# Performance work log

Hardware: AMD Instinct MI355X
Metric: run time of the kernel (lower is better)

## Reference

```python
import jax, jax.numpy as jnp
import numpy as np

H = 8        # heads
R = 8        # rank of Lambda
WWIN = 8     # topk window w
T = 2        # num_iterations


def _rotate_half(x):
    h = x.shape[-1] // 2
    return jnp.concatenate([-x[..., h:], x[..., :h]], axis=-1)


def _gelu(x):
    return jax.nn.gelu(x, approximate=False)  # torch nn.GELU default is exact erf


def _forward(target, context, Wt, bt, Wc, bc, Ws1, bs1, Ws2, bs2,
             Wa1, ba1, Wa2, ba2, Wl1, bl1, Wl2, bl2, step_sizes, Wo, bo):
    B, L, D = target.shape
    K = context.shape[1]
    HD = D // H
    u = (target @ Wt + bt).reshape(B, L, H, HD).transpose(0, 2, 1, 3)   # [B,H,L,HD]
    v = (context @ Wc + bc).reshape(B, K, H, HD).transpose(0, 2, 1, 3)  # [B,H,K,HD]

    # scored-window connectivity: first scorer layer is separable over concat([t_i, c_j])
    h1 = (target @ Ws1[:D])[:, :, None, :] + (context @ Ws1[D:])[:, None, :, :] + bs1  # [B,L,K,EH]
    scores = (_gelu(h1) @ Ws2 + bs2)[..., 0]                                           # [B,L,K]
    _, idx = jax.lax.top_k(scores, WWIN)                                               # [B,L,w]
    E = L * WWIN
    edge_j = idx.reshape(B, E)
    edge_i = jnp.broadcast_to(jnp.repeat(jnp.arange(L), WWIN)[None], (B, E))

    # per-edge learnable params R_ij = alpha_ij I + Lambda_ij Lambda_ij^T
    tf = jnp.take_along_axis(target, edge_i[..., None], axis=1)   # [B,E,D]
    cf = jnp.take_along_axis(context, edge_j[..., None], axis=1)  # [B,E,D]
    ef = jnp.concatenate([tf, cf], axis=-1)                       # [B,E,2D]
    alphas = jax.nn.softplus(_gelu(ef @ Wa1 + ba1) @ Wa2 + ba2)[..., 0]     # [B,E]
    Lam = (_gelu(ef @ Wl1 + bl1) @ Wl2 + bl2).reshape(B, E, H, R, HD)
    Lam = Lam / jnp.maximum(jnp.linalg.norm(Lam, axis=-1, keepdims=True), 1e-12)

    # relative-position rotary applied to gathered target states (model_type='SC')
    inv_freq = 1.0 / (10000.0 ** (jnp.arange(0, HD, 2, dtype=jnp.float32) / HD))
    ang = (edge_i - edge_j).astype(jnp.float32)[..., None] * inv_freq       # [B,E,HD/2]
    cos = jnp.concatenate([jnp.cos(ang), jnp.cos(ang)], -1)[:, None]        # [B,1,E,HD]
    sin = jnp.concatenate([jnp.sin(ang), jnp.sin(ang)], -1)[:, None]

    def scatter_edges(res_b, ei_b):  # res_b [H,E,HD] -> [H,L,HD]
        return jax.ops.segment_sum(res_b.transpose(1, 0, 2), ei_b,
                                   num_segments=L).transpose(1, 0, 2)

    for t in range(T):
        step = jax.nn.softplus(step_sizes[t])[None, None, :, None]          # [1,1,L,1] (max_len == L)
        u_i = jnp.take_along_axis(u, edge_i[:, None, :, None], axis=2)      # [B,H,E,HD]
        u_i = u_i * cos + _rotate_half(u_i) * sin
        v_j = jnp.take_along_axis(v, edge_j[:, None, :, None], axis=2)      # [B,H,E,HD]
        diff = u_i - v_j
        Ld = jnp.einsum('behrd,bhed->bher', Lam, diff)                      # [B,H,E,R]
        residual = alphas[:, None, :, None] * diff + jnp.einsum('bher,behrd->bhed', Ld, Lam)
        u = u - step * jax.vmap(scatter_edges)(residual, edge_i)

    y = u.transpose(0, 2, 1, 3).reshape(B, L, D) @ Wo + bo  # dropout is identity in eval
    return y


def setup_inputs() -> dict:
    key = jax.random.key(0)
    B, L, K, D, EH = 2, 2048, 2048, 512, 16
    HD = D // H
    ks = iter(jax.random.split(key, 24))

    def lin(i, o):
        return jax.random.normal(next(ks), (i, o), jnp.float32) * (1.0 / float(np.sqrt(i)))

    def bias(o):
        return jnp.zeros((o,), jnp.float32)

    return {
        'target': jax.random.normal(next(ks), (B, L, D), jnp.float32),
        'context': jax.random.normal(next(ks), (B, K, D), jnp.float32),
        'Wt': lin(D, D), 'bt': bias(D),
        'Wc': lin(D, D), 'bc': bias(D),
        'Ws1': lin(2 * D, EH), 'bs1': bias(EH),
        'Ws2': lin(EH, 1), 'bs2': bias(1),
        'Wa1': lin(2 * D, EH), 'ba1': bias(EH),
        'Wa2': lin(EH, 1), 'ba2': bias(1),
        'Wl1': lin(2 * D, EH), 'bl1': bias(EH),
        'Wl2': lin(EH, H * R * HD), 'bl2': bias(H * R * HD),
        'step_sizes': jnp.full((T, L), -2.2, jnp.float32),
        'Wo': lin(D, D), 'bo': bias(D),
    }


def reference(target, context, Wt, bt, Wc, bc, Ws1, bs1, Ws2, bs2,
              Wa1, ba1, Wa2, ba2, Wl1, bl1, Wl2, bl2, step_sizes, Wo, bo):
    return _forward(target, context, Wt, bt, Wc, bc, Ws1, bs1, Ws2, bs2,
                    Wa1, ba1, Wa2, ba2, Wl1, bl1, Wl2, bl2, step_sizes, Wo, bo)
```

## Files before the change

### kernel.cpp

```cpp
#include <hip/hip_runtime.h>
#include <math.h>

#define BB 2
#define LL 2048
#define KK 2048
#define DD 512
#define HH 8
#define HD_ 64
#define RR 8
#define WWIN 8
#define NE (LL * WWIN)

typedef __attribute__((ext_vector_type(8))) short bf16x8s;
typedef __attribute__((ext_vector_type(4))) float f32x4;

__device__ __forceinline__ float gelu_f(float x) {
    return 0.5f * x * (1.0f + erff(x * 0.70710678118654752f));
}
__device__ __forceinline__ float softplus_f(float x) {
    return (x > 20.0f) ? x : log1pf(expf(x));
}
__device__ __forceinline__ unsigned short f2bf(float f) {
    unsigned int x = __float_as_uint(f);
    x += 0x7FFFu + ((x >> 16) & 1u);
    return (unsigned short)(x >> 16);
}
__device__ __forceinline__ float bf2f(unsigned short s) {
    return __uint_as_float(((unsigned int)s) << 16);
}

#define GEMM_SMEM_BYTES 15360

__device__ __forceinline__ void gemm_bf16_body(
    const float* __restrict__ A, const float* __restrict__ W,
    const float* __restrict__ bias, float* __restrict__ C,
    int M, int N, int Kd, int bx, int by, char* smem) {
    short (*As)[40] = (short(*)[40])smem;
    short (*Bs)[40] = (short(*)[40])(smem + 128 * 40 * 2);
    const int tid = threadIdx.x;
    const int m0 = bx * 128, n0 = by * 64;
    const int wv = tid >> 6, lane = tid & 63;
    const int wm = (wv & 1) << 6, wn = (wv >> 1) << 5;
    const int l15 = lane & 15, lg = lane >> 4;

    f32x4 acc[4][2] = {};
    union S8 { bf16x8s v; short s[8]; };

    const int arow = tid >> 1, akh = (tid & 1) << 4;
    const int bk = tid >> 3, bnb = (tid & 7) << 3;

    for (int k0 = 0; k0 < Kd; k0 += 32) {
        {
            const float* ap = &A[(size_t)(m0 + arow) * Kd + k0 + akh];
            float4 f0 = *(const float4*)(ap + 0);
            float4 f1 = *(const float4*)(ap + 4);
            float4 f2 = *(const float4*)(ap + 8);
            float4 f3 = *(const float4*)(ap + 12);
            S8 s0, s1;
            s0.s[0] = f2bf(f0.x); s0.s[1] = f2bf(f0.y); s0.s[2] = f2bf(f0.z); s0.s[3] = f2bf(f0.w);
            s0.s[4] = f2bf(f1.x); s0.s[5] = f2bf(f1.y); s0.s[6] = f2bf(f1.z); s0.s[7] = f2bf(f1.w);
            s1.s[0] = f2bf(f2.x); s1.s[1] = f2bf(f2.y); s1.s[2] = f2bf(f2.z); s1.s[3] = f2bf(f2.w);
            s1.s[4] = f2bf(f3.x); s1.s[5] = f2bf(f3.y); s1.s[6] = f2bf(f3.z); s1.s[7] = f2bf(f3.w);
            *(bf16x8s*)&As[arow][akh] = s0.v;
            *(bf16x8s*)&As[arow][akh + 8] = s1.v;
        }
        {
            const float* wp = &W[(size_t)(k0 + bk) * N + n0 + bnb];
            float4 w0 = *(const float4*)(wp + 0);
            float4 w1 = *(const float4*)(wp + 4);
            Bs[bnb + 0][bk] = f2bf(w0.x);
            Bs[bnb + 1][bk] = f2bf(w0.y);
            Bs[bnb + 2][bk] = f2bf(w0.z);
            Bs[bnb + 3][bk] = f2bf(w0.w);
            Bs[bnb + 4][bk] = f2bf(w1.x);
            Bs[bnb + 5][bk] = f2bf(w1.y);
            Bs[bnb + 6][bk] = f2bf(w1.z);
            Bs[bnb + 7][bk] = f2bf(w1.w);
        }
        __syncthreads();
        bf16x8s af[4], bf[2];
#pragma unroll
        for (int mf = 0; mf < 4; ++mf)
            af[mf] = *(const bf16x8s*)&As[wm + (mf << 4) + l15][lg << 3];
#pragma unroll
        for (int nf = 0; nf < 2; ++nf)
            bf[nf] = *(const bf16x8s*)&Bs[wn + (nf << 4) + l15][lg << 3];
#pragma unroll
        for (int mf = 0; mf < 4; ++mf)
#pragma unroll
            for (int nf = 0; nf < 2; ++nf)
                acc[mf][nf] = __builtin_amdgcn_mfma_f32_16x16x32_bf16(af[mf], bf[nf], acc[mf][nf], 0, 0, 0);
        __syncthreads();
    }
    float bv[2] = {0.f, 0.f};
    if (bias) {
        bv[0] = bias[n0 + wn + l15];
        bv[1] = bias[n0 + wn + 16 + l15];
    }
#pragma unroll
    for (int mf = 0; mf < 4; ++mf)
#pragma unroll
        for (int nf = 0; nf < 2; ++nf)
#pragma unroll
            for (int j = 0; j < 4; ++j) {
                int crow = m0 + wm + (mf << 4) + (lg << 2) + j;
                int ccol = n0 + wn + (nf << 4) + l15;
                C[(size_t)crow * N + ccol] = acc[mf][nf][j] + bv[nf];
            }
}

__device__ __forceinline__ void gemm_f32_body(
    const float* __restrict__ A, const float* __restrict__ W,
    float* __restrict__ C, int M, int N, int Kd, int bx, int by, char* smem) {
    float (*As)[68] = (float(*)[68])smem;
    float (*Bs)[68] = (float(*)[68])(smem + 16 * 68 * 4);
    const int tid = threadIdx.x;
    const int m0 = bx * 64, n0 = by * 64;
    const int tx = tid & 15, ty = tid >> 4;
    const int row_a = tid >> 2, kq_a = (tid & 3) << 2;
    const int kw = tid >> 4, nq = (tid & 15) << 2;
    float acc[4][4] = {};
    for (int k0 = 0; k0 < Kd; k0 += 16) {
        float4 av = *(const float4*)&A[(size_t)(m0 + row_a) * Kd + k0 + kq_a];
        As[kq_a + 0][row_a] = av.x;
        As[kq_a + 1][row_a] = av.y;
        As[kq_a + 2][row_a] = av.z;
        As[kq_a + 3][row_a] = av.w;
        *(float4*)&Bs[kw][nq] = *(const float4*)&W[(size_t)(k0 + kw) * N + n0 + nq];
        __syncthreads();
#pragma unroll
        for (int k = 0; k < 16; ++k) {
            float4 a4 = *(const float4*)&As[k][ty << 2];
            float4 b4 = *(const float4*)&Bs[k][tx << 2];
            acc[0][0] = fmaf(a4.x, b4.x, acc[0][0]);
            acc[0][1] = fmaf(a4.x, b4.y, acc[0][1]);
            acc[0][2] = fmaf(a4.x, b4.z, acc[0][2]);
            acc[0][3] = fmaf(a4.x, b4.w, acc[0][3]);
            acc[1][0] = fmaf(a4.y, b4.x, acc[1][0]);
            acc[1][1] = fmaf(a4.y, b4.y, acc[1][1]);
            acc[1][2] = fmaf(a4.y, b4.z, acc[1][2]);
            acc[1][3] = fmaf(a4.y, b4.w, acc[1][3]);
            acc[2][0] = fmaf(a4.z, b4.x, acc[2][0]);
            acc[2][1] = fmaf(a4.z, b4.y, acc[2][1]);
            acc[2][2] = fmaf(a4.z, b4.z, acc[2][2]);
            acc[2][3] = fmaf(a4.z, b4.w, acc[2][3]);
            acc[3][0] = fmaf(a4.w, b4.x, acc[3][0]);
            acc[3][1] = fmaf(a4.w, b4.y, acc[3][1]);
            acc[3][2] = fmaf(a4.w, b4.z, acc[3][2]);
            acc[3][3] = fmaf(a4.w, b4.w, acc[3][3]);
        }
        __syncthreads();
    }
#pragma unroll
    for (int q = 0; q < 4; ++q) {
        float4 o;
        o.x = acc[q][0];
        o.y = acc[q][1];
        o.z = acc[q][2];
        o.w = acc[q][3];
        *(float4*)&C[(size_t)(m0 + (ty << 2) + q) * N + n0 + (tx << 2)] = o;
    }
}

__global__ __launch_bounds__(256) void gemms_all(
    const float* __restrict__ target, const float* __restrict__ context,
    const float* __restrict__ Wt, const float* __restrict__ bt,
    const float* __restrict__ Wc, const float* __restrict__ bc,
    const float* __restrict__ wct, const float* __restrict__ wcc,
    float* __restrict__ u, float* __restrict__ v,
    float* __restrict__ t64, float* __restrict__ c64) {
    __shared__ __align__(16) char smem[GEMM_SMEM_BYTES];
    const int bid = blockIdx.x;
    if (bid < 64) {
        gemm_f32_body(target, wct, t64, 4096, 64, 512, bid, 0, smem);
    } else if (bid < 128) {
        gemm_f32_body(context, wcc, c64, 4096, 64, 512, bid - 64, 0, smem);
    } else if (bid < 384) {
        const int r = bid - 128;
        gemm_bf16_body(target, Wt, bt, u, 4096, 512, 512, r & 31, r >> 5, smem);
    } else {
        const int r = bid - 384;
        gemm_bf16_body(context, Wc, bc, v, 4096, 512, 512, r & 31, r >> 5, smem);
    }
}

__global__ __launch_bounds__(256) void gemm_bf16(
    const float* __restrict__ A, const float* __restrict__ W,
    const float* __restrict__ bias, float* __restrict__ C,
    int M, int N, int Kd) {
    __shared__ __align__(16) char smem[GEMM_SMEM_BYTES];
    gemm_bf16_body(A, W, bias, C, M, N, Kd, blockIdx.x, blockIdx.y, smem);
}

__global__ void prep_all(const float* __restrict__ Ws1, const float* __restrict__ Wa1,
                         const float* __restrict__ Wl1,
                         const float* __restrict__ Wl2, const float* __restrict__ bl2,
                         float* __restrict__ Wct, float* __restrict__ Wcc,
                         unsigned short* __restrict__ wl2bfT,
                         float* __restrict__ rot) {
    if (blockIdx.x < 128) {
        int idx = blockIdx.x * 256 + threadIdx.x;
        int k = idx >> 6, c = idx & 63;
        float vt = 0.f, vc = 0.f;
        if (c < 16)      { vt = Ws1[k * 16 + c];        vc = Ws1[(512 + k) * 16 + c]; }
        else if (c < 32) { vt = Wa1[k * 16 + (c - 16)]; vc = Wa1[(512 + k) * 16 + (c - 16)]; }
        else if (c < 48) { vt = Wl1[k * 16 + (c - 32)]; vc = Wl1[(512 + k) * 16 + (c - 32)]; }
        Wct[idx] = vt;
        Wcc[idx] = vc;
    } else if (blockIdx.x < 144) {
        int c = (blockIdx.x - 128) * 256 + threadIdx.x;
        union U8 { bf16x8s v; unsigned short s[8]; } r0, r1, r2, r3;
#pragma unroll
        for (int k = 0; k < 8; ++k) r0.s[k] = f2bf(Wl2[(size_t)k * 4096 + c]);
#pragma unroll
        for (int k = 0; k < 8; ++k) r1.s[k] = f2bf(Wl2[(size_t)(k + 8) * 4096 + c]);
#pragma unroll
        for (int k = 0; k < 8; ++k) { r2.s[k] = 0; r3.s[k] = 0; }
        r2.s[0] = f2bf(bl2[c]);
        unsigned short* dst = &wl2bfT[(size_t)c * 32];
        *(bf16x8s*)(dst + 0)  = r0.v;
        *(bf16x8s*)(dst + 8)  = r1.v;
        *(bf16x8s*)(dst + 16) = r2.v;
        *(bf16x8s*)(dst + 24) = r3.v;
    } else {
        int idx = (blockIdx.x - 144) * 256 + threadIdx.x;
        int dlt = (idx >> 5) - 2047;
        int k = idx & 31;
        float invf = exp2f((float)k * (-13.287712379549449f / 32.0f));
        float s, c;
        sincosf((float)dlt * invf, &s, &c);
        ((float2*)rot)[idx] = make_float2(c, s);
    }
}

__global__ __launch_bounds__(256) void scores_topk(
    const float* __restrict__ t64, const float* __restrict__ c64,
    const float* __restrict__ bs1, const float* __restrict__ Ws2,
    const float* __restrict__ bs2, int* __restrict__ edge_j) {
    __shared__ float sc[KK];
    __shared__ float wvs[4];
    __shared__ int wvj[4];
    const int tid = threadIdx.x;
    const int b = blockIdx.x >> 11;
    const int i = blockIdx.x & (LL - 1);
    float tsb[16], w2[16];
    const float* tr = &t64[(size_t)(b * LL + i) * 64];
#pragma unroll
    for (int k = 0; k < 16; ++k) { tsb[k] = tr[k] + bs1[k]; w2[k] = Ws2[k]; }
    const float b2 = bs2[0];
    for (int j = tid; j < KK; j += 256) {
        const float4* cr4 = (const float4*)&c64[(size_t)(b * KK + j) * 64];
        float creg[16];
        float4 c0 = cr4[0], c1 = cr4[1], c2 = cr4[2], c3 = cr4[3];
        creg[0] = c0.x; creg[1] = c0.y; creg[2] = c0.z; creg[3] = c0.w;
        creg[4] = c1.x; creg[5] = c1.y; creg[6] = c1.z; creg[7] = c1.w;
        creg[8] = c2.x; creg[9] = c2.y; creg[10] = c2.z; creg[11] = c2.w;
        creg[12] = c3.x; creg[13] = c3.y; creg[14] = c3.z; creg[15] = c3.w;
        float s = b2;
#pragma unroll
        for (int k = 0; k < 16; ++k)
            s = fmaf(gelu_f(tsb[k] + creg[k]), w2[k], s);
        sc[j] = s;
    }
    __syncthreads();

    float ls[8];
#pragma unroll
    for (int k = 0; k < 8; ++k) ls[k] = sc[tid + (k << 8)];
    const int lane = tid & 63, wv = tid >> 6;
#pragma unroll
    for (int w = 0; w < WWIN; ++w) {
        float cs = ls[0];
        int ck = 0;
#pragma unroll
        for (int k = 1; k < 8; ++k)
            if (ls[k] > cs) { cs = ls[k]; ck = k; }
        int cj = tid + (ck << 8);
#pragma unroll
        for (int m = 1; m < 64; m <<= 1) {
            float os = __shfl_xor(cs, m);
            int oj = __shfl_xor(cj, m);
            if (os > cs || (os == cs && oj < cj)) { cs = os; cj = oj; }
        }
        if (lane == 0) { wvs[wv] = cs; wvj[wv] = cj; }
        __syncthreads();
        float bsv = wvs[0];
        int bjv = wvj[0];
#pragma unroll
        for (int q = 1; q < 4; ++q) {
            float qs = wvs[q];
            int qj = wvj[q];
            if (qs > bsv || (qs == bsv && qj < bjv)) { bsv = qs; bjv = qj; }
        }
        if (tid == 0) edge_j[(size_t)(b * LL + i) * WWIN + w] = bjv;
        {
            const bool own = (bjv & 255) == tid;
            const int bk = bjv >> 8;
#pragma unroll
            for (int k = 0; k < 8; ++k)
                if (own && bk == k) ls[k] = -INFINITY;
        }
        __syncthreads();
    }
}

__global__ __launch_bounds__(256) void edge_params(
    const float* __restrict__ t64, const float* __restrict__ c64,
    const int* __restrict__ edge_j,
    const float* __restrict__ bl1, const float* __restrict__ ba1,
    const float* __restrict__ Wa2, const float* __restrict__ ba2,
    unsigned short* __restrict__ h16bf, float* __restrict__ alpha) {
    int idx = blockIdx.x * 256 + threadIdx.x;
    if (idx >= BB * NE) return;
    int b = idx >> 14;
    int i = (idx & (NE - 1)) >> 3;
    int j = edge_j[idx];
    const float* tr = &t64[(size_t)(b * LL + i) * 64];
    const float* cr = &c64[(size_t)(b * KK + j) * 64];
    union U8 { bf16x8s v; unsigned short s[8]; } o0, o1, o2, o3;
    float s = ba2[0];
#pragma unroll
    for (int k = 0; k < 8; ++k) {
        o0.s[k] = f2bf(gelu_f(tr[32 + k] + cr[32 + k] + bl1[k]));
        s = fmaf(gelu_f(tr[16 + k] + cr[16 + k] + ba1[k]), Wa2[k], s);
    }
#pragma unroll
    for (int k = 8; k < 16; ++k) {
        o1.s[k - 8] = f2bf(gelu_f(tr[32 + k] + cr[32 + k] + bl1[k]));
        s = fmaf(gelu_f(tr[16 + k] + cr[16 + k] + ba1[k]), Wa2[k], s);
    }
#pragma unroll
    for (int k = 0; k < 8; ++k) { o2.s[k] = 0; o3.s[k] = 0; }
    o2.s[0] = 0x3F80;
    unsigned short* dst = &h16bf[(size_t)idx * 32];
    *(bf16x8s*)(dst + 0)  = o0.v;
    *(bf16x8s*)(dst + 8)  = o1.v;
    *(bf16x8s*)(dst + 16) = o2.v;
    *(bf16x8s*)(dst + 24) = o3.v;
    alpha[idx] = softplus_f(s);
}

__global__ __launch_bounds__(256, 3) void iterate_k(
    float* __restrict__ u, const float* __restrict__ v,
    const int* __restrict__ edge_j, const float* __restrict__ alpha,
    const unsigned short* __restrict__ h16bf,
    const unsigned short* __restrict__ wl2bfT,
    const float* __restrict__ rotT,
    const float* __restrict__ step_sizes) {
    __shared__ unsigned short lam_s[32 * 520];
    __shared__ float alphs[32];
    __shared__ int ejs[32];
    __shared__ float dts[4][64];
    const int tid = threadIdx.x;
    const int h = blockIdx.y, b = blockIdx.z;
    const int i0 = blockIdx.x << 2;
    const int e0 = b * NE + (i0 << 3);

    if (tid < 32) { ejs[tid] = edge_j[e0 + tid]; alphs[tid] = alpha[e0 + tid]; }

    const int wv = tid >> 6, lane = tid & 63;
    const int l15 = lane & 15, lg = lane >> 4;

    {
        const int mt = wv & 1;
        const int rbase = (wv >> 1) << 2;
        bf16x8s afrag = *(const bf16x8s*)&h16bf[(size_t)(e0 + (mt << 4) + l15) * 32 + (lg << 3)];
        const unsigned short* wbase = &wl2bfT[((size_t)(h * 512 + (rbase << 6) + l15)) * 32 + (lg << 3)];
#pragma unroll
        for (int g = 0; g < 4; ++g) {
            f32x4 a0 = {0.f, 0.f, 0.f, 0.f}, a1 = a0, a2 = a0, a3 = a0;
            const unsigned short* wg = wbase + g * 512;
            a0 = __builtin_amdgcn_mfma_f32_16x16x32_bf16(afrag, *(const bf16x8s*)(wg + 0),    a0, 0, 0, 0);
            a1 = __builtin_amdgcn_mfma_f32_16x16x32_bf16(afrag, *(const bf16x8s*)(wg + 2048), a1, 0, 0, 0);
            a2 = __builtin_amdgcn_mfma_f32_16x16x32_bf16(afrag, *(const bf16x8s*)(wg + 4096), a2, 0, 0, 0);
            a3 = __builtin_amdgcn_mfma_f32_16x16x32_bf16(afrag, *(const bf16x8s*)(wg + 6144), a3, 0, 0, 0);
            const int d = (g << 4) + l15;
#pragma unroll
            for (int j = 0; j < 4; ++j) {
                const int e = (mt << 4) + (lg << 2) + j;
                uint2 pk;
                pk.x = (unsigned int)f2bf(a0[j]) | ((unsigned int)f2bf(a1[j]) << 16);
                pk.y = (unsigned int)f2bf(a2[j]) | ((unsigned int)f2bf(a3[j]) << 16);
                *(uint2*)&lam_s[e * 520 + (d << 3) + rbase] = pk;
            }
        }
    }
    __syncthreads();

    const int i = i0 + wv;
    const size_t urow = ((size_t)(b * LL + i)) * DD + h * HD_ + lane;
    float u_d = u[urow];
    const float st0 = softplus_f(step_sizes[i]);
    const float st1 = softplus_f(step_sizes[LL + i]);

    const bool up32 = (lane & 32) != 0;
    const bool up16 = (lane & 16) != 0;
    const bool up8  = (lane & 8) != 0;
    const bool up4  = (lane & 4) != 0;
    const bool up2  = (lane & 2) != 0;
    const bool up1  = (lane & 1) != 0;

    float lamr[8][8];
#pragma unroll
    for (int w = 0; w < 8; ++w) {
        union U8 { bf16x8s v; unsigned short s[8]; } lv;
        lv.v = *(const bf16x8s*)&lam_s[((wv << 3) + w) * 520 + (lane << 3)];
#pragma unroll
        for (int r = 0; r < 8; ++r) lamr[w][r] = bf2f(lv.s[r]);
    }

    float inv_ss;
    {
        float q[32];
#pragma unroll
        for (int wp = 0; wp < 4; ++wp)
#pragma unroll
            for (int r = 0; r < 8; ++r) {
                float plo = lamr[wp][r] * lamr[wp][r];
                float phi = lamr[wp + 4][r] * lamr[wp + 4][r];
                float recv = __shfl_xor(up32 ? plo : phi, 32);
                q[(wp << 3) + r] = (up32 ? phi : plo) + recv;
            }
#pragma unroll
        for (int j = 0; j < 16; ++j) {
            float lo = q[j], hi = q[j + 16];
            float recv = __shfl_xor(up16 ? lo : hi, 16);
            q[j] = (up16 ? hi : lo) + recv;
        }
#pragma unroll
        for (int j = 0; j < 8; ++j) {
            float lo = q[j], hi = q[j + 8];
            float recv = __shfl_xor(up8 ? lo : hi, 8);
            q[j] = (up8 ? hi : lo) + recv;
        }
#pragma unroll
        for (int j = 0; j < 4; ++j) {
            float lo = q[j], hi = q[j + 4];
            float recv = __shfl_xor(up4 ? lo : hi, 4);
            q[j] = (up4 ? hi : lo) + recv;
        }
#pragma unroll
        for (int j = 0; j < 2; ++j) {
            float lo = q[j], hi = q[j + 2];
            float recv = __shfl_xor(up2 ? lo : hi, 2);
            q[j] = (up2 ? hi : lo) + recv;
        }
        {
            float lo = q[0], hi = q[1];
            float recv = __shfl_xor(up1 ? lo : hi, 1);
            q[0] = (up1 ? hi : lo) + recv;
        }
        inv_ss = 1.0f / fmaxf(q[0], 1e-24f);
    }

    const int k31 = lane & 31;
    float vw[8], cw[8], sw[8], aw[8];
#pragma unroll
    for (int w = 0; w < 8; ++w) {
        const int le = (wv << 3) + w;
        const int j = ejs[le];
        aw[w] = alphs[le];
        vw[w] = v[((size_t)(b * KK + j)) * DD + h * HD_ + lane];
        float2 rc = ((const float2*)rotT)[((size_t)(i - j + 2047) << 5) + k31];
        cw[w] = rc.x;
        sw[w] = rc.y;
    }

#pragma unroll
    for (int t = 0; t < 2; ++t) {
        float upv = __shfl_xor(u_d, 32);
        float rotb = (lane < 32) ? -upv : upv;
        float resid = 0.0f;
        float q[32];
#pragma unroll
        for (int wp = 0; wp < 4; ++wp) {
            float dlo = fmaf(u_d, cw[wp], rotb * sw[wp]) - vw[wp];
            float dhi = fmaf(u_d, cw[wp + 4], rotb * sw[wp + 4]) - vw[wp + 4];
            resid = fmaf(aw[wp], dlo, resid);
            resid = fmaf(aw[wp + 4], dhi, resid);
#pragma unroll
            for (int r = 0; r < 8; ++r) {
                float plo = lamr[wp][r] * dlo;
                float phi = lamr[wp + 4][r] * dhi;
                float recv = __shfl_xor(up32 ? plo : phi, 32);
                q[(wp << 3) + r] = (up32 ? phi : plo) + recv;
            }
        }
#pragma unroll
        for (int j = 0; j < 16; ++j) {
            float lo = q[j], hi = q[j + 16];
            float recv = __shfl_xor(up16 ? lo : hi, 16);
            q[j] = (up16 ? hi : lo) + recv;
        }
#pragma unroll
        for (int j = 0; j < 8; ++j) {
            float lo = q[j], hi = q[j + 8];
            float recv = __shfl_xor(up8 ? lo : hi, 8);
            q[j] = (up8 ? hi : lo) + recv;
        }
#pragma unroll
        for (int j = 0; j < 4; ++j) {
            float lo = q[j], hi = q[j + 4];
            float recv = __shfl_xor(up4 ? lo : hi, 4);
            q[j] = (up4 ? hi : lo) + recv;
        }
#pragma unroll
        for (int j = 0; j < 2; ++j) {
            float lo = q[j], hi = q[j + 2];
            float recv = __shfl_xor(up2 ? lo : hi, 2);
            q[j] = (up2 ? hi : lo) + recv;
        }
        {
            float lo = q[0], hi = q[1];
            float recv = __shfl_xor(up1 ? lo : hi, 1);
            q[0] = (up1 ? hi : lo) + recv;
        }
        dts[wv][lane] = q[0] * inv_ss;
#pragma unroll
        for (int w = 0; w < 8; ++w) {
            float4 da = *(const float4*)&dts[wv][(w << 3)];
            float4 db = *(const float4*)&dts[wv][(w << 3) + 4];
            resid = fmaf(da.x, lamr[w][0], resid);
            resid = fmaf(da.y, lamr[w][1], resid);
            resid = fmaf(da.z, lamr[w][2], resid);
            resid = fmaf(da.w, lamr[w][3], resid);
            resid = fmaf(db.x, lamr[w][4], resid);
            resid = fmaf(db.y, lamr[w][5], resid);
            resid = fmaf(db.z, lamr[w][6], resid);
            resid = fmaf(db.w, lamr[w][7], resid);
        }
        u_d = fmaf((t == 0) ? -st0 : -st1, resid, u_d);
    }
    u[urow] = u_d;
}

extern "C" void kernel_launch(void* const* d_in, const int* in_sizes, int n_in,
                              void* d_out, int out_size, void* d_ws, size_t ws_size,
                              hipStream_t stream) {
    (void)in_sizes; (void)n_in; (void)out_size; (void)ws_size;
    const float* target     = (const float*)d_in[0];
    const float* context    = (const float*)d_in[1];
    const float* Wt         = (const float*)d_in[2];
    const float* bt         = (const float*)d_in[3];
    const float* Wc         = (const float*)d_in[4];
    const float* bc         = (const float*)d_in[5];
    const float* Ws1        = (const float*)d_in[6];
    const float* bs1        = (const float*)d_in[7];
    const float* Ws2        = (const float*)d_in[8];
    const float* bs2        = (const float*)d_in[9];
    const float* Wa1        = (const float*)d_in[10];
    const float* ba1        = (const float*)d_in[11];
    const float* Wa2        = (const float*)d_in[12];
    const float* ba2        = (const float*)d_in[13];
    const float* Wl1        = (const float*)d_in[14];
    const float* bl1        = (const float*)d_in[15];
    const float* Wl2        = (const float*)d_in[16];
    const float* bl2        = (const float*)d_in[17];
    const float* step_sizes = (const float*)d_in[18];
    const float* Wo         = (const float*)d_in[19];
    const float* bo         = (const float*)d_in[20];
    float* out = (float*)d_out;

    float* ws = (float*)d_ws;
    float* u    = ws;
    float* v    = ws + 2097152;
    float* t64  = ws + 4194304;
    float* c64  = ws + 4456448;
    unsigned short* h16bf = (unsigned short*)(ws + 4718592);
    float* alph = ws + 5242880;
    int*   ej   = (int*)(ws + 5275648);
    float* wct  = ws + 5308416;
    float* wcc  = ws + 5341184;
    unsigned short* wl2bfT = (unsigned short*)(ws + 5373952);
    float* rotT = out;

    prep_all<<<dim3(656), dim3(256), 0, stream>>>(
        Ws1, Wa1, Wl1, Wl2, bl2, wct, wcc, wl2bfT, rotT);

    gemms_all<<<dim3(640), dim3(256), 0, stream>>>(
        target, context, Wt, bt, Wc, bc, wct, wcc, u, v, t64, c64);

    scores_topk<<<dim3(BB * LL), dim3(256), 0, stream>>>(t64, c64, bs1, Ws2, bs2, ej);

    edge_params<<<dim3(BB * NE / 256), dim3(256), 0, stream>>>(t64, c64, ej, bl1, ba1, Wa2, ba2, h16bf, alph);

    iterate_k<<<dim3(LL / 4, HH, BB), dim3(256), 0, stream>>>(u, v, ej, alph, h16bf, wl2bfT, rotT, step_sizes);

    gemm_bf16<<<dim3(32, 8), dim3(256), 0, stream>>>(u, Wo, bo, out, 4096, 512, 512);
}
```

Before: 286.9 us.

## Move u/v projection GEMMs into the scores/top-k launch to overlap them

```diff
diff --git a/kernel.cpp b/kernel.cpp
--- a/kernel.cpp
+++ b/kernel.cpp
@@ -162,26 +162,15 @@
     }
 }
 
-__global__ __launch_bounds__(256) void gemms_all(
+__global__ __launch_bounds__(256) void gemms_f32(
     const float* __restrict__ target, const float* __restrict__ context,
-    const float* __restrict__ Wt, const float* __restrict__ bt,
-    const float* __restrict__ Wc, const float* __restrict__ bc,
     const float* __restrict__ wct, const float* __restrict__ wcc,
-    float* __restrict__ u, float* __restrict__ v,
     float* __restrict__ t64, float* __restrict__ c64) {
-    __shared__ __align__(16) char smem[GEMM_SMEM_BYTES];
-    const int bid = blockIdx.x;
-    if (bid < 64) {
-        gemm_f32_body(target, wct, t64, 4096, 64, 512, bid, 0, smem);
-    } else if (bid < 128) {
-        gemm_f32_body(context, wcc, c64, 4096, 64, 512, bid - 64, 0, smem);
-    } else if (bid < 384) {
-        const int r = bid - 128;
-        gemm_bf16_body(target, Wt, bt, u, 4096, 512, 512, r & 31, r >> 5, smem);
-    } else {
-        const int r = bid - 384;
-        gemm_bf16_body(context, Wc, bc, v, 4096, 512, 512, r & 31, r >> 5, smem);
-    }
+    __shared__ __align__(16) char smem[16 * 68 * 4 * 2];
+    if (blockIdx.x < 64)
+        gemm_f32_body(target, wct, t64, 4096, 64, 512, blockIdx.x, 0, smem);
+    else
+        gemm_f32_body(context, wcc, c64, 4096, 64, 512, blockIdx.x - 64, 0, smem);
 }
 
 __global__ __launch_bounds__(256) void gemm_bf16(
@@ -233,16 +222,15 @@
     }
 }
 
-__global__ __launch_bounds__(256) void scores_topk(
+__device__ __forceinline__ void scores_topk_body(
     const float* __restrict__ t64, const float* __restrict__ c64,
     const float* __restrict__ bs1, const float* __restrict__ Ws2,
-    const float* __restrict__ bs2, int* __restrict__ edge_j) {
-    __shared__ float sc[KK];
-    __shared__ float wvs[4];
-    __shared__ int wvj[4];
+    const float* __restrict__ bs2, int* __restrict__ edge_j,
+    int b, int i, char* smem) {
+    float* sc = (float*)smem;
+    float* wvs = (float*)(smem + 8192);
+    int* wvj = (int*)(smem + 8192 + 16);
     const int tid = threadIdx.x;
-    const int b = blockIdx.x >> 11;
-    const int i = blockIdx.x & (LL - 1);
     float tsb[16], w2[16];
     const float* tr = &t64[(size_t)(b * LL + i) * 64];
 #pragma unroll
@@ -301,6 +289,28 @@
                 if (own && bk == k) ls[k] = -INFINITY;
         }
         __syncthreads();
+    }
+}
+
+__global__ __launch_bounds__(256) void scores_uv(
+    const float* __restrict__ target, const float* __restrict__ context,
+    const float* __restrict__ Wt, const float* __restrict__ bt,
+    const float* __restrict__ Wc, const float* __restrict__ bc,
+    float* __restrict__ u, float* __restrict__ v,
+    const float* __restrict__ t64, const float* __restrict__ c64,
+    const float* __restrict__ bs1, const float* __restrict__ Ws2,
+    const float* __restrict__ bs2, int* __restrict__ edge_j) {
+    __shared__ __align__(16) char smem[GEMM_SMEM_BYTES];
+    const int bid = blockIdx.x;
+    if (bid < 256) {
+        gemm_bf16_body(target, Wt, bt, u, 4096, 512, 512, bid & 31, bid >> 5, smem);
+    } else if (bid < 512) {
+        const int r = bid - 256;
+        gemm_bf16_body(context, Wc, bc, v, 4096, 512, 512, r & 31, r >> 5, smem);
+    } else {
+        const int sid = bid - 512;
+        scores_topk_body(t64, c64, bs1, Ws2, bs2, edge_j,
+                         sid >> 11, sid & (LL - 1), smem);
     }
 }
 
@@ -577,10 +587,11 @@
     prep_all<<<dim3(656), dim3(256), 0, stream>>>(
         Ws1, Wa1, Wl1, Wl2, bl2, wct, wcc, wl2bfT, rotT);
 
-    gemms_all<<<dim3(640), dim3(256), 0, stream>>>(
-        target, context, Wt, bt, Wc, bc, wct, wcc, u, v, t64, c64);
-
-    scores_topk<<<dim3(BB * LL), dim3(256), 0, stream>>>(t64, c64, bs1, Ws2, bs2, ej);
+    gemms_f32<<<dim3(128), dim3(256), 0, stream>>>(
+        target, context, wct, wcc, t64, c64);
+
+    scores_uv<<<dim3(4608), dim3(256), 0, stream>>>(
+        target, context, Wt, bt, Wc, bc, u, v, t64, c64, bs1, Ws2, bs2, ej);
 
     edge_params<<<dim3(BB * NE / 256), dim3(256), 0, stream>>>(t64, c64, ej, bl1, ba1, Wa2, ba2, h16bf, alph);
 
```

New measurement: 306.1 us. 6.7% more time.
